# Performance work log

Measured on AMD Instinct MI355X. Metric: run time of the kernel, lower is better.

The kernel has to match this reference:

```python
import jax, jax.numpy as jnp
import numpy as np

MAX_SHIFT = 2
SMOOTH = 1.0

def setup_inputs() -> dict:
    key = jax.random.key(0)
    k1, k2 = jax.random.split(key)
    # predicted probabilities in [0,1)
    inputs = jax.random.uniform(k1, (64, 1, 512, 512), dtype=jnp.float32)
    # soft targets (the original accepts any float mask); uniform works as a stand-in
    targets = jax.random.uniform(k2, (64, 1, 512, 512), dtype=jnp.float32)
    return {"inputs": inputs, "targets": targets}

def reference(inputs, targets):
    # all (shift_y, shift_x) pairs from the 5x5 nested loop
    shifts = jnp.array(
        [(sy, sx)
         for sx in range(-MAX_SHIFT, MAX_SHIFT + 1)
         for sy in range(-MAX_SHIFT, MAX_SHIFT + 1)],
        dtype=jnp.int32,
    )  # [25, 2]

    # global sums; targets.sum() is invariant under roll but kept per the original math
    i_sum = inputs.sum()
    t_sum = targets.sum()

    def dice_loss(shift):
        st = jnp.roll(targets, (shift[0], shift[1]), axis=(2, 3))
        intersection = jnp.sum(inputs * st)
        return 1.0 - (2.0 * intersection + SMOOTH) / (i_sum + t_sum + SMOOTH)

    losses = jax.vmap(dice_loss)(shifts)  # [25]
    return jnp.min(losses)
```

## Files before the change

### kernel.cpp

```cpp
#include <hip/hip_runtime.h>

#define H 512
#define W 512
#define TILE 64
#define TG_ROWS 68
#define TG_C4 18
#define TG_STRIDE 76

__device__ __forceinline__ float wave_sum_dpp(float x) {
#define DPP_STEP(ctrl)                                                          \
    x += __int_as_float(__builtin_amdgcn_update_dpp(                            \
        0, __float_as_int(x), (ctrl), 0xF, 0xF, true))
    DPP_STEP(0x111);
    DPP_STEP(0x112);
    DPP_STEP(0x114);
    DPP_STEP(0x118);
    DPP_STEP(0x142);
    DPP_STEP(0x143);
#undef DPP_STEP
    return x;
}

__global__ __launch_bounds__(256, 8)
void dice_partial(const float* __restrict__ in, const float* __restrict__ tg,
                  float* __restrict__ ws, int nblocks) {
    __shared__ float tgs[TG_ROWS * TG_STRIDE];
    __shared__ float warr[4][32];

    const int bx = blockIdx.x, by = blockIdx.y, b = blockIdx.z;
    const int x0 = bx * TILE, y0 = by * TILE;
    const size_t ibase = (size_t)b * (H * W);
    const int tid = threadIdx.x;
    const int wave = tid >> 6, lane = tid & 63;

    const int x40 = x0 >> 2;
    for (int idx = tid; idx < TG_ROWS * TG_C4; idx += 256) {
        const int rr = idx / TG_C4;
        const int c4 = idx - rr * TG_C4;
        const int gy  = (y0 - 2 + rr) & (H - 1);
        const int gx4 = (x40 - 1 + c4) & (W / 4 - 1);
        const float4 v = *reinterpret_cast<const float4*>(tg + ibase + (size_t)gy * W + (size_t)gx4 * 4);
        *reinterpret_cast<float4*>(&tgs[rr * TG_STRIDE + c4 * 4]) = v;
    }

    const int r = tid >> 2;
    const int sseg = tid & 3;
    const float* ip = in + ibase + (size_t)(y0 + r) * W + x0 + sseg * 16;
    float iv[16];
#pragma unroll
    for (int k = 0; k < 4; ++k) {
        const float4 v = *reinterpret_cast<const float4*>(ip + 4 * k);
        iv[4*k+0] = v.x; iv[4*k+1] = v.y; iv[4*k+2] = v.z; iv[4*k+3] = v.w;
    }
    {
        float isum = 0.f;
#pragma unroll
        for (int k = 0; k < 16; ++k) isum += iv[k];
        isum = wave_sum_dpp(isum);
        if (lane == 63) warr[wave][25] = isum;
    }

    __syncthreads();

#pragma unroll
    for (int t = 0; t < 5; ++t) {
        float wrow[24];
        const float* base = &tgs[(r + t) * TG_STRIDE + sseg * 16];
#pragma unroll
        for (int k = 0; k < 6; ++k) {
            const float4 v = *reinterpret_cast<const float4*>(base + 4 * k);
            wrow[4*k+0] = v.x; wrow[4*k+1] = v.y; wrow[4*k+2] = v.z; wrow[4*k+3] = v.w;
        }

        float acc[5];
#pragma unroll
        for (int ss = 0; ss < 5; ++ss) acc[ss] = 0.f;
#pragma unroll
        for (int ss = 0; ss < 5; ++ss) {
#pragma unroll
            for (int px = 0; px < 16; ++px)
                acc[ss] += iv[px] * wrow[px + 6 - ss];
        }

        if (t == 2) {
            float tsum = 0.f;
#pragma unroll
            for (int px = 0; px < 16; ++px) tsum += wrow[px + 4];
            tsum = wave_sum_dpp(tsum);
            if (lane == 63) warr[wave][26] = tsum;
        }

#pragma unroll
        for (int ss = 0; ss < 5; ++ss) {
            const float v = wave_sum_dpp(acc[ss]);
            if (lane == 63) warr[wave][t * 5 + ss] = v;
        }
    }

    __syncthreads();
    if (tid < 27) {
        const float s = warr[0][tid] + warr[1][tid] + warr[2][tid] + warr[3][tid];
        const int bid = (b * (int)gridDim.y + by) * (int)gridDim.x + bx;
        ws[tid * nblocks + bid] = s;
    }
}

__global__ __launch_bounds__(256)
void dice_reduce(const float* __restrict__ ws, float* __restrict__ tot, int nblocks) {
    __shared__ float red[4];
    const int k = blockIdx.x;
    const int tid = threadIdx.x;
    const float* p = ws + (size_t)k * nblocks;

    float s = 0.f;
    for (int i = tid; i < nblocks; i += 256) s += p[i];
    s = wave_sum_dpp(s);
    if ((tid & 63) == 63) red[tid >> 6] = s;
    __syncthreads();
    if (tid == 0) tot[k] = red[0] + red[1] + red[2] + red[3];
}

__global__ void dice_out(const float* __restrict__ tot, float* __restrict__ out) {
    const int tid = threadIdx.x;
    float v = (tid < 25) ? tot[tid] : -1e30f;
#pragma unroll
    for (int off = 32; off; off >>= 1) v = fmaxf(v, __shfl_down(v, off, 64));
    if (tid == 0) {
        const float denom = tot[25] + tot[26] + 1.0f;
        out[0] = 1.0f - (2.0f * v + 1.0f) / denom;
    }
}

extern "C" void kernel_launch(void* const* d_in, const int* in_sizes, int n_in,
                              void* d_out, int out_size, void* d_ws, size_t ws_size,
                              hipStream_t stream) {
    const float* inputs  = (const float*)d_in[0];
    const float* targets = (const float*)d_in[1];
    float* out = (float*)d_out;
    float* ws  = (float*)d_ws;

    const int B = in_sizes[0] / (H * W);
    const int tx = W / TILE, ty = H / TILE;
    const int nblocks = B * tx * ty;

    float* tot = ws + (size_t)27 * nblocks;

    dim3 grid(tx, ty, B);
    dice_partial<<<grid, 256, 0, stream>>>(inputs, targets, ws, nblocks);
    dice_reduce<<<27, 256, 0, stream>>>(ws, tot, nblocks);
    dice_out<<<1, 64, 0, stream>>>(tot, out);
}
```

Baseline: 47.12 us.

## Replace LDS-tiled shift correlation with per-wave row strips and lane shuffles

Each wave now handles a full-width strip of four rows, with each lane owning eight columns. Target rows are loaded straight from global memory, and the horizontal halo comes from cross-lane shuffles instead of a shared-memory tile. All 25 shift accumulators are held in registers, and the 8 target rows are reused across the 4 input rows, which removes the LDS staging and the block-wide sync. Block indices are also swizzled across the grid, and launch bounds drop to 4 blocks per CU. The cost is higher register pressure from 25 accumulators plus 32 input values, which may reduce occupancy, and each strip rereads 4 halo rows from global memory.

After: 41.20 us. 1.14x faster.

```diff
diff --git a/kernel.cpp b/kernel.cpp
--- a/kernel.cpp
+++ b/kernel.cpp
@@ -2,10 +2,6 @@
 
 #define H 512
 #define W 512
-#define TILE 64
-#define TG_ROWS 68
-#define TG_C4 18
-#define TG_STRIDE 76
 
 __device__ __forceinline__ float wave_sum_dpp(float x) {
 #define DPP_STEP(ctrl)                                                          \
@@ -21,86 +17,95 @@
     return x;
 }
 
-__global__ __launch_bounds__(256, 8)
+__device__ __forceinline__ float4 ld4(const float* p) {
+    return *reinterpret_cast<const float4*>(p);
+}
+
+__global__ __launch_bounds__(256, 4)
 void dice_partial(const float* __restrict__ in, const float* __restrict__ tg,
                   float* __restrict__ ws, int nblocks) {
-    __shared__ float tgs[TG_ROWS * TG_STRIDE];
     __shared__ float warr[4][32];
 
-    const int bx = blockIdx.x, by = blockIdx.y, b = blockIdx.z;
-    const int x0 = bx * TILE, y0 = by * TILE;
-    const size_t ibase = (size_t)b * (H * W);
-    const int tid = threadIdx.x;
+    const int tid  = threadIdx.x;
     const int wave = tid >> 6, lane = tid & 63;
 
-    const int x40 = x0 >> 2;
-    for (int idx = tid; idx < TG_ROWS * TG_C4; idx += 256) {
-        const int rr = idx / TG_C4;
-        const int c4 = idx - rr * TG_C4;
-        const int gy  = (y0 - 2 + rr) & (H - 1);
-        const int gx4 = (x40 - 1 + c4) & (W / 4 - 1);
-        const float4 v = *reinterpret_cast<const float4*>(tg + ibase + (size_t)gy * W + (size_t)gx4 * 4);
-        *reinterpret_cast<float4*>(&tgs[rr * TG_STRIDE + c4 * 4]) = v;
+    const int bid = blockIdx.x;
+    const int wrk = (bid & 7) * (nblocks >> 3) + (bid >> 3);
+
+    const int q  = wrk * 4 + wave;
+    const int b  = q >> 7;
+    const int y0 = (q & 127) << 2;
+    const size_t ibase = (size_t)b * (H * W);
+
+    const int laneL = (lane + 63) & 63;
+    const int laneR = (lane + 1) & 63;
+
+    const float* ibp = in + ibase + (size_t)y0 * W + lane * 8;
+    float iv[4][8];
+    float isum = 0.f;
+#pragma unroll
+    for (int yi = 0; yi < 4; ++yi) {
+        const float4 a = ld4(ibp + (size_t)yi * W);
+        const float4 c = ld4(ibp + (size_t)yi * W + 4);
+        iv[yi][0] = a.x; iv[yi][1] = a.y; iv[yi][2] = a.z; iv[yi][3] = a.w;
+        iv[yi][4] = c.x; iv[yi][5] = c.y; iv[yi][6] = c.z; iv[yi][7] = c.w;
+#pragma unroll
+        for (int j = 0; j < 8; ++j) isum += iv[yi][j];
     }
 
-    const int r = tid >> 2;
-    const int sseg = tid & 3;
-    const float* ip = in + ibase + (size_t)(y0 + r) * W + x0 + sseg * 16;
-    float iv[16];
+    float acc[25];
 #pragma unroll
-    for (int k = 0; k < 4; ++k) {
-        const float4 v = *reinterpret_cast<const float4*>(ip + 4 * k);
-        iv[4*k+0] = v.x; iv[4*k+1] = v.y; iv[4*k+2] = v.z; iv[4*k+3] = v.w;
-    }
-    {
-        float isum = 0.f;
-#pragma unroll
-        for (int k = 0; k < 16; ++k) isum += iv[k];
-        isum = wave_sum_dpp(isum);
-        if (lane == 63) warr[wave][25] = isum;
-    }
-
-    __syncthreads();
+    for (int k = 0; k < 25; ++k) acc[k] = 0.f;
+    float tsum = 0.f;
 
 #pragma unroll
-    for (int t = 0; t < 5; ++t) {
-        float wrow[24];
-        const float* base = &tgs[(r + t) * TG_STRIDE + sseg * 16];
+    for (int t = 0; t < 8; ++t) {
+        const int yt = (y0 - 2 + t) & (H - 1);
+        const float* tp = tg + ibase + (size_t)yt * W + lane * 8;
+
+        float tw[12];
+        const float4 a = ld4(tp);
+        const float4 c = ld4(tp + 4);
+        tw[2] = a.x; tw[3] = a.y; tw[4] = a.z; tw[5] = a.w;
+        tw[6] = c.x; tw[7] = c.y; tw[8] = c.z; tw[9] = c.w;
+        tw[0]  = __shfl(tw[8], laneL, 64);
+        tw[1]  = __shfl(tw[9], laneL, 64);
+        tw[10] = __shfl(tw[2], laneR, 64);
+        tw[11] = __shfl(tw[3], laneR, 64);
+
+        if (t >= 2 && t <= 5) {
 #pragma unroll
-        for (int k = 0; k < 6; ++k) {
-            const float4 v = *reinterpret_cast<const float4*>(base + 4 * k);
-            wrow[4*k+0] = v.x; wrow[4*k+1] = v.y; wrow[4*k+2] = v.z; wrow[4*k+3] = v.w;
-        }
-
-        float acc[5];
-#pragma unroll
-        for (int ss = 0; ss < 5; ++ss) acc[ss] = 0.f;
-#pragma unroll
-        for (int ss = 0; ss < 5; ++ss) {
-#pragma unroll
-            for (int px = 0; px < 16; ++px)
-                acc[ss] += iv[px] * wrow[px + 6 - ss];
-        }
-
-        if (t == 2) {
-            float tsum = 0.f;
-#pragma unroll
-            for (int px = 0; px < 16; ++px) tsum += wrow[px + 4];
-            tsum = wave_sum_dpp(tsum);
-            if (lane == 63) warr[wave][26] = tsum;
+            for (int j = 0; j < 8; ++j) tsum += tw[j + 2];
         }
 
 #pragma unroll
-        for (int ss = 0; ss < 5; ++ss) {
-            const float v = wave_sum_dpp(acc[ss]);
-            if (lane == 63) warr[wave][t * 5 + ss] = v;
+        for (int yi = 0; yi < 4; ++yi) {
+            const int sy = yi + 2 - t;
+            if (sy < -2 || sy > 2) continue;
+#pragma unroll
+            for (int sx = -2; sx <= 2; ++sx) {
+#pragma unroll
+                for (int j = 0; j < 8; ++j)
+                    acc[(sy + 2) * 5 + (sx + 2)] += iv[yi][j] * tw[j + 2 - sx];
+            }
         }
+    }
+
+#pragma unroll
+    for (int k = 0; k < 25; ++k) {
+        const float v = wave_sum_dpp(acc[k]);
+        if (lane == 63) warr[wave][k] = v;
+    }
+    {
+        const float v = wave_sum_dpp(isum);
+        if (lane == 63) warr[wave][25] = v;
+        const float u = wave_sum_dpp(tsum);
+        if (lane == 63) warr[wave][26] = u;
     }
 
     __syncthreads();
     if (tid < 27) {
         const float s = warr[0][tid] + warr[1][tid] + warr[2][tid] + warr[3][tid];
-        const int bid = (b * (int)gridDim.y + by) * (int)gridDim.x + bx;
         ws[tid * nblocks + bid] = s;
     }
 }
@@ -140,13 +145,11 @@
     float* ws  = (float*)d_ws;
 
     const int B = in_sizes[0] / (H * W);
-    const int tx = W / TILE, ty = H / TILE;
-    const int nblocks = B * tx * ty;
+    const int nblocks = B * (H / 4) / 4;
 
     float* tot = ws + (size_t)27 * nblocks;
 
-    dim3 grid(tx, ty, B);
-    dice_partial<<<grid, 256, 0, stream>>>(inputs, targets, ws, nblocks);
+    dice_partial<<<nblocks, 256, 0, stream>>>(inputs, targets, ws, nblocks);
     dice_reduce<<<27, 256, 0, stream>>>(ws, tot, nblocks);
     dice_out<<<1, 64, 0, stream>>>(tot, out);
 }
```

## Use taller 64x128 tiles with 512 threads and per-wave partials

Applied to the files above, without the earlier changes.

Doubles the tile height to 128 rows with 512-thread blocks, which cuts the halo overhead of the staged target rows from 68/64 to 132/128. The grid is flattened, and a swizzle spreads consecutive block ids across batch images. The final shared-memory cross-wave combine and its second barrier are dropped, so each wave writes its partial sums straight to the workspace. In exchange the reduce kernel reads eight times more partial entries, and the larger blocks may lower occupancy.

New measurement: 49.45 us. 5.0% more time.

```diff
diff --git a/kernel.cpp b/kernel.cpp
--- a/kernel.cpp
+++ b/kernel.cpp
@@ -2,10 +2,12 @@
 
 #define H 512
 #define W 512
-#define TILE 64
-#define TG_ROWS 68
+#define TILE_W 64
+#define TILE_H 128
+#define TG_ROWS (TILE_H + 4)
 #define TG_C4 18
 #define TG_STRIDE 76
+#define NWAVE 8
 
 __device__ __forceinline__ float wave_sum_dpp(float x) {
 #define DPP_STEP(ctrl)                                                          \
@@ -21,26 +23,39 @@
     return x;
 }
 
-__global__ __launch_bounds__(256, 8)
+__device__ __forceinline__ float4 ld4(const float* p) {
+    return *reinterpret_cast<const float4*>(p);
+}
+
+__global__ __launch_bounds__(512, 8)
 void dice_partial(const float* __restrict__ in, const float* __restrict__ tg,
                   float* __restrict__ ws, int nblocks) {
-    __shared__ float tgs[TG_ROWS * TG_STRIDE];
-    __shared__ float warr[4][32];
+    __shared__ __align__(16) float tgs[TG_ROWS * TG_STRIDE];
 
-    const int bx = blockIdx.x, by = blockIdx.y, b = blockIdx.z;
-    const int x0 = bx * TILE, y0 = by * TILE;
-    const size_t ibase = (size_t)b * (H * W);
-    const int tid = threadIdx.x;
+    const int tid  = threadIdx.x;
     const int wave = tid >> 6, lane = tid & 63;
 
+    const int bid = blockIdx.x;
+    const int wrk = (bid & 7) * (nblocks >> 3) + (bid >> 3);
+
+    const int b    = wrk >> 5;
+    const int tile = wrk & 31;
+    const int y0   = (tile >> 3) * TILE_H;
+    const int x0   = (tile & 7) * TILE_W;
+    const size_t ibase = (size_t)b * (H * W);
+
     const int x40 = x0 >> 2;
-    for (int idx = tid; idx < TG_ROWS * TG_C4; idx += 256) {
-        const int rr = idx / TG_C4;
-        const int c4 = idx - rr * TG_C4;
-        const int gy  = (y0 - 2 + rr) & (H - 1);
-        const int gx4 = (x40 - 1 + c4) & (W / 4 - 1);
-        const float4 v = *reinterpret_cast<const float4*>(tg + ibase + (size_t)gy * W + (size_t)gx4 * 4);
-        *reinterpret_cast<float4*>(&tgs[rr * TG_STRIDE + c4 * 4]) = v;
+#pragma unroll
+    for (int ii = 0; ii < 5; ++ii) {
+        const int idx = tid + ii * 512;
+        if (idx < TG_ROWS * TG_C4) {
+            const int rr = idx / TG_C4;
+            const int c4 = idx - rr * TG_C4;
+            const int gy  = (y0 - 2 + rr) & (H - 1);
+            const int gx4 = (x40 - 1 + c4) & (W / 4 - 1);
+            const float4 v = ld4(tg + ibase + (size_t)gy * W + (size_t)gx4 * 4);
+            *reinterpret_cast<float4*>(&tgs[rr * TG_STRIDE + c4 * 4]) = v;
+        }
     }
 
     const int r = tid >> 2;
@@ -49,26 +64,25 @@
     float iv[16];
 #pragma unroll
     for (int k = 0; k < 4; ++k) {
-        const float4 v = *reinterpret_cast<const float4*>(ip + 4 * k);
+        const float4 v = ld4(ip + 4 * k);
         iv[4*k+0] = v.x; iv[4*k+1] = v.y; iv[4*k+2] = v.z; iv[4*k+3] = v.w;
     }
-    {
-        float isum = 0.f;
+    float isum = 0.f;
 #pragma unroll
-        for (int k = 0; k < 16; ++k) isum += iv[k];
-        isum = wave_sum_dpp(isum);
-        if (lane == 63) warr[wave][25] = isum;
-    }
+    for (int k = 0; k < 16; ++k) isum += iv[k];
 
     __syncthreads();
 
+    const int wb = bid * NWAVE + wave;
+
+    float tsum = 0.f;
 #pragma unroll
     for (int t = 0; t < 5; ++t) {
         float wrow[24];
         const float* base = &tgs[(r + t) * TG_STRIDE + sseg * 16];
 #pragma unroll
         for (int k = 0; k < 6; ++k) {
-            const float4 v = *reinterpret_cast<const float4*>(base + 4 * k);
+            const float4 v = ld4(base + 4 * k);
             wrow[4*k+0] = v.x; wrow[4*k+1] = v.y; wrow[4*k+2] = v.z; wrow[4*k+3] = v.w;
         }
 
@@ -83,37 +97,34 @@
         }
 
         if (t == 2) {
-            float tsum = 0.f;
 #pragma unroll
             for (int px = 0; px < 16; ++px) tsum += wrow[px + 4];
-            tsum = wave_sum_dpp(tsum);
-            if (lane == 63) warr[wave][26] = tsum;
         }
 
 #pragma unroll
         for (int ss = 0; ss < 5; ++ss) {
             const float v = wave_sum_dpp(acc[ss]);
-            if (lane == 63) warr[wave][t * 5 + ss] = v;
+            if (lane == 63) ws[(size_t)(t * 5 + ss) * (nblocks * NWAVE) + wb] = v;
         }
     }
 
-    __syncthreads();
-    if (tid < 27) {
-        const float s = warr[0][tid] + warr[1][tid] + warr[2][tid] + warr[3][tid];
-        const int bid = (b * (int)gridDim.y + by) * (int)gridDim.x + bx;
-        ws[tid * nblocks + bid] = s;
+    {
+        const float v = wave_sum_dpp(isum);
+        if (lane == 63) ws[(size_t)25 * (nblocks * NWAVE) + wb] = v;
+        const float u = wave_sum_dpp(tsum);
+        if (lane == 63) ws[(size_t)26 * (nblocks * NWAVE) + wb] = u;
     }
 }
 
 __global__ __launch_bounds__(256)
-void dice_reduce(const float* __restrict__ ws, float* __restrict__ tot, int nblocks) {
+void dice_reduce(const float* __restrict__ ws, float* __restrict__ tot, int nent) {
     __shared__ float red[4];
     const int k = blockIdx.x;
     const int tid = threadIdx.x;
-    const float* p = ws + (size_t)k * nblocks;
+    const float* p = ws + (size_t)k * nent;
 
     float s = 0.f;
-    for (int i = tid; i < nblocks; i += 256) s += p[i];
+    for (int i = tid; i < nent; i += 256) s += p[i];
     s = wave_sum_dpp(s);
     if ((tid & 63) == 63) red[tid >> 6] = s;
     __syncthreads();
@@ -140,13 +151,12 @@
     float* ws  = (float*)d_ws;
 
     const int B = in_sizes[0] / (H * W);
-    const int tx = W / TILE, ty = H / TILE;
-    const int nblocks = B * tx * ty;
+    const int nblocks = B * 32;
+    const int nent = nblocks * NWAVE;
 
-    float* tot = ws + (size_t)27 * nblocks;
+    float* tot = ws + (size_t)27 * nent;
 
-    dim3 grid(tx, ty, B);
-    dice_partial<<<grid, 256, 0, stream>>>(inputs, targets, ws, nblocks);
-    dice_reduce<<<27, 256, 0, stream>>>(ws, tot, nblocks);
+    dice_partial<<<nblocks, 512, 0, stream>>>(inputs, targets, ws, nblocks);
+    dice_reduce<<<27, 256, 0, stream>>>(ws, tot, nent);
     dice_out<<<1, 64, 0, stream>>>(tot, out);
 }
```
